# Optimization experiments

Measured on AMD Instinct MI355X. Metric: run time of the kernel, lower is better.

## Reference

```python
import jax, jax.numpy as jnp
import numpy as np

EPS = 1e-5

def mean_variance_norm(x):
    # x: [b,c,h,w]; torch .var(dim=2) on flattened spatial is UNBIASED (n-1)
    b, c, h, w = x.shape
    n = h * w
    mean = jnp.mean(x, axis=(2, 3), keepdims=True)
    var = jnp.sum((x - mean) ** 2, axis=(2, 3), keepdims=True) / (n - 1) + EPS
    return (x - mean) / jnp.sqrt(var)

def conv1x1(x, W, b):
    # 1x1 conv == channel-mixing matmul. W: [out_c, in_c], b: [out_c]
    return jnp.einsum('oc,bchw->bohw', W, x) + b[None, :, None, None]

def setup_inputs() -> dict:
    key = jax.random.key(0)
    ks = jax.random.split(key, 10)
    C = 512
    shp = (4, C, 64, 64)
    std = 1.0 / np.sqrt(C)
    return {
        'content': jax.random.normal(ks[0], shp, jnp.float32),
        'style': jax.random.normal(ks[1], shp, jnp.float32),
        'Wf': jax.random.normal(ks[2], (C, C), jnp.float32) * std,
        'bf': jax.random.normal(ks[3], (C,), jnp.float32) * 0.01,
        'Wg': jax.random.normal(ks[4], (C, C), jnp.float32) * std,
        'bg': jax.random.normal(ks[5], (C,), jnp.float32) * 0.01,
        'Wh': jax.random.normal(ks[6], (C, C), jnp.float32) * std,
        'bh': jax.random.normal(ks[7], (C,), jnp.float32) * 0.01,
        'Wo': jax.random.normal(ks[8], (C, C), jnp.float32) * std,
        'bo': jax.random.normal(ks[9], (C,), jnp.float32) * 0.01,
    }

def reference(content, style, Wf, bf, Wg, bg, Wh, bh, Wo, bo):
    b, c, h, w = content.shape
    hw = h * w
    F = conv1x1(mean_variance_norm(content), Wf, bf).reshape(b, c, hw)  # queries
    G = conv1x1(mean_variance_norm(style), Wg, bg).reshape(b, c, hw)    # keys
    H = conv1x1(style, Wh, bh).reshape(b, c, hw)                        # values
    # S[b,n,m] = sum_c F[b,c,n] * G[b,c,m]  (unscaled attention scores)
    S = jnp.einsum('bcn,bcm->bnm', F, G)
    S = jax.nn.softmax(S, axis=-1)
    # O[b,c,n] = sum_m H[b,c,m] * S[b,n,m]
    O = jnp.einsum('bcm,bnm->bcn', H, S).reshape(b, c, h, w)
    O = conv1x1(O, Wo, bo)
    return O + content
```

## Files before the change

### kernel.cpp

```cpp
#include <hip/hip_runtime.h>

#define C 512
#define HW 4096
#define EPSV 1e-5f

typedef _Float16 fp16x8 __attribute__((ext_vector_type(8)));
typedef _Float16 fp16x4 __attribute__((ext_vector_type(4)));
typedef float f32x4 __attribute__((ext_vector_type(4)));

#define OFF_MC    (0)
#define OFF_RC    (8192)
#define OFF_MS    (16384)
#define OFF_RS    (24576)
#define OFF_BETAF (32768)
#define OFF_V     (40960)
#define OFF_BZ    (49152)
#define OFF_T     (65536)
#define OFF_SP    (131072)
#define OFF_A     (OFF_SP + 2097152)
#define OFF_WZ    (OFF_A + 1048576)
#define OFF_XCT   (OFF_WZ + 1048576)
#define OFF_XST   (OFF_XCT + 16777216)
#define OFF_KT    (OFF_XST + 16777216)
#define OFF_HM    (OFF_KT + 16777216)
#define OFF_ML    (OFF_HM + 16777216)
#define OFF_S     (OFF_ML + 8388608)

#define FT_IDX(n, c) ((((size_t)((n) >> 4) * 16 + ((c) >> 5)) * 512) + \
                      ((((c) >> 3) & 3) * 128) + (((n) & 15) * 8) + ((c) & 7))

#define SFT_IDX(n, m) ((((size_t)((n) >> 4) * 128 + ((m) >> 5)) * 512) + \
                       ((((m) >> 3) & 3) * 128) + (((n) & 15) * 8) + ((m) & 7))



__global__ void transpose_stats_kernel(const float* __restrict__ xc, const float* __restrict__ xs,
                                       char* __restrict__ ws)
{
    int bx = blockIdx.x;
    int tensor = bx >> 11, b = (bx >> 9) & 3, c0 = ((bx >> 6) & 7) * 64, n0 = (bx & 63) * 64;
    const float* src = tensor ? xs : xc;
    _Float16* dst = (_Float16*)(ws + (tensor ? OFF_XST : OFF_XCT));
    float2* part = (float2*)(ws + OFF_SP);

    __shared__ _Float16 tile[64][72];
    __shared__ float pS[64][16], pSS[64][16];

    int tid = threadIdx.x, w = tid >> 6, lane = tid & 63, cq = lane >> 4, l16 = lane & 15;
    #pragma unroll
    for (int k = 0; k < 4; k++) {
        int cr = w * 16 + k * 4 + cq;
        int nf = l16 * 4;
        float4 v = *(const float4*)(src + ((size_t)(b * C + c0 + cr)) * HW + n0 + nf);
        pS[cr][l16] = v.x + v.y + v.z + v.w;
        pSS[cr][l16] = v.x * v.x + v.y * v.y + v.z * v.z + v.w * v.w;
        tile[nf][cr] = (_Float16)v.x; tile[nf + 1][cr] = (_Float16)v.y;
        tile[nf + 2][cr] = (_Float16)v.z; tile[nf + 3][cr] = (_Float16)v.w;
    }
    __syncthreads();
    if (tid < 64) {
        float S = 0.f, SS = 0.f;
        #pragma unroll
        for (int j = 0; j < 16; j++) { S += pS[tid][j]; SS += pSS[tid][j]; }
        part[((size_t)(n0 >> 6)) * 4096 + (tensor * 4 + b) * 512 + c0 + tid] =
            make_float2(S, SS);
    }
    _Float16* dstB = dst + (size_t)b * HW * C;
    #pragma unroll
    for (int i = 0; i < 2; i++) {
        int g = tid + i * 256, row = g >> 3, c8 = (g & 7) * 8;
        int n = n0 + row, c = c0 + c8;
        *(fp16x8*)&dstB[FT_IDX(n, c)] = *(const fp16x8*)&tile[row][c8];
    }
}

__global__ void finalize_stats_kernel(char* __restrict__ ws)
{
    int ch = blockIdx.x * 256 + threadIdx.x;
    const float2* part = (const float2*)(ws + OFF_SP);
    float S = 0.f, SS = 0.f;
    for (int k = 0; k < 64; k++) { float2 v = part[(size_t)k * 4096 + ch]; S += v.x; SS += v.y; }
    int tensor = ch >> 11, rem = ch & 2047;
    float m = S / (float)HW;
    float var = (SS - S * m) / (float)(HW - 1) + EPSV;
    ((float*)(ws + (tensor ? OFF_MS : OFF_MC)))[rem] = m;
    ((float*)(ws + (tensor ? OFF_RS : OFF_RC)))[rem] = rsqrtf(var);
}

__global__ void precompute_kernel(const float* __restrict__ Wf, const float* __restrict__ Wg,
                                  const float* __restrict__ Wo, const float* __restrict__ Wh,
                                  char* __restrict__ ws)
{
    float* A = (float*)(ws + OFF_A);
    _Float16* Wz16 = (_Float16*)(ws + OFF_WZ);
    int bx = blockIdx.x, t = threadIdx.x;
    bool isA = bx < 256;
    int r0 = (isA ? bx : bx - 256) * 2;
    float a00 = 0.f, a01 = 0.f, a10 = 0.f, a11 = 0.f;
    for (int k = 0; k < C; k++) {
        float r0v, r1v, c0v, c1v;
        if (isA) {
            r0v = Wf[k * C + r0]; r1v = Wf[k * C + r0 + 1];
            c0v = Wg[k * C + t];  c1v = Wg[k * C + t + 256];
        } else {
            r0v = Wo[r0 * C + k]; r1v = Wo[(r0 + 1) * C + k];
            c0v = Wh[k * C + t];  c1v = Wh[k * C + t + 256];
        }
        a00 += r0v * c0v; a01 += r0v * c1v;
        a10 += r1v * c0v; a11 += r1v * c1v;
    }
    if (isA) {
        A[r0 * C + t] = a00;       A[r0 * C + t + 256] = a01;
        A[(r0 + 1) * C + t] = a10; A[(r0 + 1) * C + t + 256] = a11;
    } else {
        Wz16[FT_IDX(r0, t)] = (_Float16)a00;
        Wz16[FT_IDX(r0, t + 256)] = (_Float16)a01;
        Wz16[FT_IDX(r0 + 1, t)] = (_Float16)a10;
        Wz16[FT_IDX(r0 + 1, t + 256)] = (_Float16)a11;
    }
}

__global__ void __launch_bounds__(256) vecprep_kernel(const float* __restrict__ Wf,
                                                      const float* __restrict__ bf,
                                                      const float* __restrict__ Wo,
                                                      const float* __restrict__ bh,
                                                      char* __restrict__ ws)
{
    const float* mc = (const float*)(ws + OFF_MC);
    const float* rc = (const float*)(ws + OFF_RC);
    float* betaf = (float*)(ws + OFF_BETAF);
    float* bz = (float*)(ws + OFF_BZ);

    int o = blockIdx.x * 4 + (threadIdx.x >> 6);
    int lane = threadIdx.x & 63;
    float acc = 0.f;
    if (o < 2048) {
        int b = o >> 9, co = o & 511;
        const float* wr = Wf + (size_t)co * C + lane * 8;
        const float* mp = mc + b * C + lane * 8;
        const float* rp = rc + b * C + lane * 8;
        #pragma unroll
        for (int e = 0; e < 8; e++) acc += wr[e] * mp[e] * rp[e];
    } else {
        int co = o - 2048;
        const float* wr = Wo + (size_t)co * C + lane * 8;
        const float* bp = bh + lane * 8;
        #pragma unroll
        for (int e = 0; e < 8; e++) acc += wr[e] * bp[e];
    }
    acc += __shfl_xor(acc, 1);
    acc += __shfl_xor(acc, 2);
    acc += __shfl_xor(acc, 4);
    acc += __shfl_xor(acc, 8);
    acc += __shfl_xor(acc, 16);
    acc += __shfl_xor(acc, 32);
    if (lane == 0) {
        if (o < 2048) betaf[o] = bf[o & 511] - acc;
        else bz[o - 2048] = acc;
    }
}

__global__ void __launch_bounds__(256) scaleA_kernel(char* __restrict__ ws)
{
    const float* __restrict__ A = (const float*)(ws + OFF_A);
    const float* __restrict__ rc = (const float*)(ws + OFF_RC);
    const float* __restrict__ rs = (const float*)(ws + OFF_RS);
    _Float16* __restrict__ As = (_Float16*)(ws + OFF_SP);

    __shared__ float At[16][516];
    __shared__ float rsl[512];
    __shared__ float rcl[16];

    int bx = blockIdx.x;
    int b = bx >> 5, r16 = bx & 31;
    int r0 = r16 * 16;
    int t = threadIdx.x;

    rsl[t] = rs[b * C + t];
    rsl[t + 256] = rs[b * C + t + 256];
    if (t < 16) rcl[t] = rc[b * C + r0 + t];
    {
        int row = t >> 4, cb = (t & 15) * 32;
        const float* src = A + (size_t)(r0 + row) * C + cb;
        #pragma unroll
        for (int k = 0; k < 8; k++) {
            float4 v = *(const float4*)(src + k * 4);
            At[row][cb + k * 4] = v.x; At[row][cb + k * 4 + 1] = v.y;
            At[row][cb + k * 4 + 2] = v.z; At[row][cb + k * 4 + 3] = v.w;
        }
    }
    __syncthreads();

    _Float16* AsB = As + (size_t)b * 262144 + (size_t)r16 * 8192;
    #pragma unroll
    for (int round = 0; round < 4; round++) {
        int flat = round * 2048 + t * 8;
        int cb4 = flat >> 9, rem = flat & 511;
        int low6 = rem >> 3;
        int q = low6 >> 4, l16 = low6 & 15;
        int cbase = cb4 * 32 + q * 8;
        float rcv = rcl[l16];
        fp16x8 o;
        #pragma unroll
        for (int e = 0; e < 8; e++)
            o[e] = (_Float16)(At[l16][cbase + e] * rcv * rsl[cbase + e]);
        *(fp16x8*)&AsB[flat] = o;
    }
}

__global__ void __launch_bounds__(256) precompute_v_kernel(const float* __restrict__ Wg,
                                                           char* __restrict__ ws)
{
    const float* betaf = (const float*)(ws + OFF_BETAF);
    const float* rs = (const float*)(ws + OFF_RS);
    float* v = (float*)(ws + OFF_V);

    __shared__ float bet[512];
    __shared__ float Wgt[64][68];
    __shared__ float pacc[4][64];
    __shared__ float rsl[64];

    int bx = blockIdx.x;
    int b = bx >> 3, j0 = (bx & 7) * 64;
    int t = threadIdx.x;

    bet[t] = betaf[b * C + t];
    bet[t + 256] = betaf[b * C + t + 256];
    if (t < 64) rsl[t] = rs[b * C + j0 + t];

    int j = t & 63, g = t >> 6;
    float acc = 0.f;
    for (int ch = 0; ch < 8; ch++) {
        __syncthreads();
        {
            int row = t >> 2, cq = (t & 3) * 16;
            const float* src = Wg + (size_t)(ch * 64 + row) * C + j0 + cq;
            #pragma unroll
            for (int k = 0; k < 4; k++) {
                float4 w4 = *(const float4*)(src + k * 4);
                Wgt[row][cq + k * 4] = w4.x; Wgt[row][cq + k * 4 + 1] = w4.y;
                Wgt[row][cq + k * 4 + 2] = w4.z; Wgt[row][cq + k * 4 + 3] = w4.w;
            }
        }
        __syncthreads();
        #pragma unroll
        for (int r2 = 0; r2 < 16; r2++) {
            int col = g * 16 + r2;
            acc += bet[ch * 64 + col] * Wgt[col][j];
        }
    }
    pacc[g][j] = acc;
    __syncthreads();
    if (t < 64)
        v[b * C + j0 + t] = rsl[t] * (pacc[0][t] + pacc[1][t] + pacc[2][t] + pacc[3][t]);
}

__global__ void __launch_bounds__(256) prep_gemm_kernel(char* __restrict__ ws)
{
    const _Float16* __restrict__ As = (const _Float16*)(ws + OFF_SP);
    const _Float16* __restrict__ Wz16 = (const _Float16*)(ws + OFF_WZ);
    const float* __restrict__ bz = (const float*)(ws + OFF_BZ);
    const _Float16* __restrict__ xsT = (const _Float16*)(ws + OFF_XST);
    _Float16* __restrict__ Kt = (_Float16*)(ws + OFF_KT);
    _Float16* __restrict__ Hp = (_Float16*)(ws + OFF_HM);

    int bx = blockIdx.x;
    int b = bx & 3, rest = bx >> 2;
    int r128 = rest >> 5, mb = rest & 31;
    int r0 = r128 * 128, m0 = mb * 128;
    int w = threadIdx.x >> 6, lane = threadIdx.x & 63, q = lane >> 4, l16 = lane & 15;
    int wr = (w & 1) * 64, wm = (w >> 1) * 64;
    bool isK = (r0 < 512);
    int rbase = (isK ? r0 : r0 - 512) + wr;

    f32x4 zz = {0.f, 0.f, 0.f, 0.f};
    f32x4 acc[4][4];
    #pragma unroll
    for (int rt = 0; rt < 4; rt++)
        #pragma unroll
        for (int mt = 0; mt < 4; mt++) acc[rt][mt] = zz;

    const _Float16* ap = (isK ? As + (size_t)b * 262144 : Wz16)
                         + (size_t)(rbase >> 4) * 8192 + q * 128 + l16 * 8;
    const _Float16* xb = xsT + (size_t)b * HW * C
                             + (size_t)((m0 + wm) >> 4) * 8192 + q * 128 + l16 * 8;

    for (int ks = 0; ks < 16; ks++) {
        fp16x8 afr[4], bfr[4];
        #pragma unroll
        for (int rt = 0; rt < 4; rt++)
            afr[rt] = *(const fp16x8*)(ap + (size_t)rt * 8192 + ks * 512);
        #pragma unroll
        for (int mt = 0; mt < 4; mt++)
            bfr[mt] = *(const fp16x8*)(xb + (size_t)(mt * 16 + ks) * 512);
        #pragma unroll
        for (int rt = 0; rt < 4; rt++)
            #pragma unroll
            for (int mt = 0; mt < 4; mt++)
                acc[rt][mt] = __builtin_amdgcn_mfma_f32_16x16x32_f16(afr[rt], bfr[mt], acc[rt][mt], 0, 0, 0);
    }

    if (isK) {
        _Float16* KtB = Kt + (size_t)b * HW * C;
        #pragma unroll
        for (int rt = 0; rt < 4; rt++)
            #pragma unroll
            for (int mt = 0; mt < 4; mt++) {
                int m = m0 + wm + mt * 16 + l16;
                int cb = r0 + wr + rt * 16 + q * 4;
                fp16x4 h;
                h[0] = (_Float16)acc[rt][mt][0]; h[1] = (_Float16)acc[rt][mt][1];
                h[2] = (_Float16)acc[rt][mt][2]; h[3] = (_Float16)acc[rt][mt][3];
                *(fp16x4*)&KtB[FT_IDX(m, cb)] = h;
            }
    } else {
        _Float16* HpB = Hp + (size_t)b * 2097152;
        #pragma unroll
        for (int rt = 0; rt < 4; rt++) {
            float bzv[4];
            #pragma unroll
            for (int reg = 0; reg < 4; reg++) bzv[reg] = bz[rbase + rt * 16 + q * 4 + reg];
            #pragma unroll
            for (int mt = 0; mt < 4; mt++) {
                int m = m0 + wm + mt * 16 + l16;
                int mbase = (m >> 3) * 128 + (m & 7);
                #pragma unroll
                for (int reg = 0; reg < 4; reg++) {
                    int co = rbase + rt * 16 + q * 4 + reg;
                    HpB[(size_t)(co >> 4) * 65536 + mbase + (co & 15) * 8] =
                        (_Float16)(acc[rt][mt][reg] + bzv[reg]);
                }
            }
        }
    }
}

__global__ void t_kernel(char* __restrict__ ws)
{
    const float* v = (const float*)(ws + OFF_V);
    const _Float16* __restrict__ xsT = (const _Float16*)(ws + OFF_XST);
    float* tG = (float*)(ws + OFF_T);
    int bx = blockIdx.x;
    int b = bx >> 6, mb = bx & 63;
    int tid = threadIdx.x, w = tid >> 6, lane = tid & 63, q = lane >> 4, l16 = lane & 15;
    int M16 = mb * 4 + w;
    const _Float16* p = xsT + (size_t)b * HW * C + (size_t)M16 * 8192 + q * 128 + l16 * 8;
    const float* vp = v + b * C + q * 8;
    float acc = 0.f;
    #pragma unroll
    for (int st = 0; st < 16; st++) {
        fp16x8 xv = *(const fp16x8*)(p + st * 512);
        float4 v0 = *(const float4*)(vp + st * 32);
        float4 v1 = *(const float4*)(vp + st * 32 + 4);
        acc += (float)xv[0] * v0.x + (float)xv[1] * v0.y + (float)xv[2] * v0.z + (float)xv[3] * v0.w
             + (float)xv[4] * v1.x + (float)xv[5] * v1.y + (float)xv[6] * v1.z + (float)xv[7] * v1.w;
    }
    acc += __shfl_xor(acc, 16);
    acc += __shfl_xor(acc, 32);
    if (q == 0) tG[b * HW + M16 * 16 + l16] = acc;
}

__global__ void __launch_bounds__(256, 4) qk_kernel(char* __restrict__ ws)
{
    const _Float16* __restrict__ xcT = (const _Float16*)(ws + OFF_XCT);
    const _Float16* __restrict__ Kt = (const _Float16*)(ws + OFF_KT);
    const float* __restrict__ tG = (const float*)(ws + OFF_T);
    float2* __restrict__ ML = (float2*)(ws + OFF_ML);
    _Float16* __restrict__ Sg = (_Float16*)(ws + OFF_S);

    int bx = blockIdx.x;
    int b = (bx >> 1) & 3, mhi = bx & 1;
    int rest = bx >> 3, mlo = rest & 15, ntile = rest >> 4;
    int m0 = (mhi * 16 + mlo) * 128, n0 = ntile * 128;
    int tid = threadIdx.x, w = tid >> 6, lane = tid & 63, q = lane >> 4, l16 = lane & 15;
    int wn = (w & 1) * 64, wm = (w >> 1) * 64;

    __shared__ char lbuf[36864];
    _Float16* Ax0 = (_Float16*)lbuf;
    _Float16* Bx0 = (_Float16*)(lbuf + 16384);

    int st = tid >> 5, so = (tid & 31) * 16;
    const _Float16* gA = xcT + (size_t)b * HW * C + ((size_t)(n0 >> 4) + st) * 8192 + so;
    const _Float16* gB = Kt + (size_t)b * HW * C + ((size_t)(m0 >> 4) + st) * 8192 + so;

    {
        fp16x8 a0 = *(const fp16x8*)(gA);
        fp16x8 a1 = *(const fp16x8*)(gA + 8);
        fp16x8 b0 = *(const fp16x8*)(gB);
        fp16x8 b1 = *(const fp16x8*)(gB + 8);
        *(fp16x8*)&Ax0[tid * 16] = a0; *(fp16x8*)&Ax0[tid * 16 + 8] = a1;
        *(fp16x8*)&Bx0[tid * 16] = b0; *(fp16x8*)&Bx0[tid * 16 + 8] = b1;
    }
    __syncthreads();

    f32x4 zz = {0.f, 0.f, 0.f, 0.f};
    f32x4 acc[4][4];
    #pragma unroll
    for (int nt = 0; nt < 4; nt++)
        #pragma unroll
        for (int mt = 0; mt < 4; mt++) acc[nt][mt] = zz;

    int aoff = ((wn >> 4)) * 512 + q * 128 + l16 * 8;
    int boff = ((wm >> 4)) * 512 + q * 128 + l16 * 8;

    for (int ks = 0; ks < 16; ks++) {
        int buf = ks & 1;
        _Float16* Axc = Ax0 + buf * 4096;
        _Float16* Bxc = Bx0 + buf * 4096;
        fp16x8 a0n, a1n, b0n, b1n;
        if (ks < 15) {
            a0n = *(const fp16x8*)(gA + (ks + 1) * 512);
            a1n = *(const fp16x8*)(gA + (ks + 1) * 512 + 8);
            b0n = *(const fp16x8*)(gB + (ks + 1) * 512);
            b1n = *(const fp16x8*)(gB + (ks + 1) * 512 + 8);
        }

        fp16x8 afr[4], bfr[4];
        #pragma unroll
        for (int nt = 0; nt < 4; nt++)
            afr[nt] = *(const fp16x8*)&Axc[aoff + nt * 512];
        #pragma unroll
        for (int mt = 0; mt < 4; mt++)
            bfr[mt] = *(const fp16x8*)&Bxc[boff + mt * 512];
        #pragma unroll
        for (int nt = 0; nt < 4; nt++)
            #pragma unroll
            for (int mt = 0; mt < 4; mt++)
                acc[nt][mt] = __builtin_amdgcn_mfma_f32_16x16x32_f16(afr[nt], bfr[mt], acc[nt][mt], 0, 0, 0);

        if (ks < 15) {
            _Float16* Axn = Ax0 + (buf ^ 1) * 4096;
            _Float16* Bxn = Bx0 + (buf ^ 1) * 4096;
            *(fp16x8*)&Axn[tid * 16] = a0n; *(fp16x8*)&Axn[tid * 16 + 8] = a1n;
            *(fp16x8*)&Bxn[tid * 16] = b0n; *(fp16x8*)&Bxn[tid * 16 + 8] = b1n;
        }
        __syncthreads();
    }

    float tv[4];
    #pragma unroll
    for (int mt = 0; mt < 4; mt++) tv[mt] = tG[b * HW + m0 + wm + mt * 16 + l16];
    #pragma unroll
    for (int nt = 0; nt < 4; nt++)
        #pragma unroll
        for (int mt = 0; mt < 4; mt++)
            #pragma unroll
            for (int reg = 0; reg < 4; reg++) acc[nt][mt][reg] += tv[mt];

    float rm[4][4], sum[4][4];
    #pragma unroll
    for (int nt = 0; nt < 4; nt++)
        #pragma unroll
        for (int reg = 0; reg < 4; reg++)
            rm[nt][reg] = fmaxf(fmaxf(acc[nt][0][reg], acc[nt][1][reg]),
                                fmaxf(acc[nt][2][reg], acc[nt][3][reg]));
    #pragma unroll
    for (int s = 1; s < 16; s <<= 1)
        #pragma unroll
        for (int nt = 0; nt < 4; nt++)
            #pragma unroll
            for (int reg = 0; reg < 4; reg++)
                rm[nt][reg] = fmaxf(rm[nt][reg], __shfl_xor(rm[nt][reg], s));
    #pragma unroll
    for (int nt = 0; nt < 4; nt++)
        #pragma unroll
        for (int reg = 0; reg < 4; reg++) sum[nt][reg] = 0.f;
    #pragma unroll
    for (int nt = 0; nt < 4; nt++)
        #pragma unroll
        for (int mt = 0; mt < 4; mt++)
            #pragma unroll
            for (int reg = 0; reg < 4; reg++) {
                float pv = __expf(acc[nt][mt][reg] - rm[nt][reg]);
                acc[nt][mt][reg] = pv;
                sum[nt][reg] += pv;
            }
    #pragma unroll
    for (int s = 1; s < 16; s <<= 1)
        #pragma unroll
        for (int nt = 0; nt < 4; nt++)
            #pragma unroll
            for (int reg = 0; reg < 4; reg++)
                sum[nt][reg] += __shfl_xor(sum[nt][reg], s);

    int tl = (m0 + wm) >> 6;
    if (l16 == 0) {
        #pragma unroll
        for (int nt = 0; nt < 4; nt++)
            #pragma unroll
            for (int reg = 0; reg < 4; reg++)
                ML[((size_t)(b * HW + n0 + wn + nt * 16 + q * 4 + reg)) * 64 + tl] =
                    make_float2(rm[nt][reg], sum[nt][reg]);
    }

    _Float16 (*Pl)[64][72] = (_Float16(*)[64][72])lbuf;
    #pragma unroll
    for (int nt = 0; nt < 4; nt++)
        #pragma unroll
        for (int mt = 0; mt < 4; mt++)
            #pragma unroll
            for (int reg = 0; reg < 4; reg++)
                Pl[w][nt * 16 + q * 4 + reg][mt * 16 + l16] = (_Float16)acc[nt][mt][reg];
    __syncthreads();
    _Float16* SgB = Sg + (size_t)b * 16777216;
    #pragma unroll
    for (int i = 0; i < 8; i++) {
        int row = i * 8 + (lane >> 3), c8 = (lane & 7) * 8;
        int n = n0 + wn + row, m = m0 + wm + c8;
        *(fp16x8*)&SgB[SFT_IDX(n, m)] = *(const fp16x8*)&Pl[w][row][c8];
    }
}

__global__ void __launch_bounds__(256) scale_kernel(char* __restrict__ ws)
{
    const float* __restrict__ mlf0 = (const float*)(ws + OFF_ML);
    float* __restrict__ Scl = (float*)(ws + OFF_XCT);
    __shared__ float mlv[64][129];
    __shared__ float Ms[64], Li[64];

    int g0 = blockIdx.x * 64;
    int tid = threadIdx.x;
    const float* mlf = mlf0 + (size_t)g0 * 128;

    #pragma unroll
    for (int i = 0; i < 8; i++) {
        int f4 = i * 256 + tid;
        int row = f4 >> 5, c4 = (f4 & 31) * 4;
        float4 v = *(const float4*)(mlf + row * 128 + c4);
        mlv[row][c4] = v.x; mlv[row][c4 + 1] = v.y;
        mlv[row][c4 + 2] = v.z; mlv[row][c4 + 3] = v.w;
    }
    __syncthreads();
    if (tid < 64) {
        float M = -1e30f;
        #pragma unroll
        for (int k = 0; k < 64; k++) M = fmaxf(M, mlv[tid][k * 2]);
        float L = 0.f;
        #pragma unroll
        for (int k = 0; k < 64; k++) L += mlv[tid][k * 2 + 1] * __expf(mlv[tid][k * 2] - M);
        Ms[tid] = M; Li[tid] = 1.f / L;
    }
    __syncthreads();
    int b = g0 >> 12, nbase = g0 & 4095;
    float* sp = Scl + (size_t)b * 262144 + nbase;
    int row = tid & 63, tsub = tid >> 6;
    #pragma unroll
    for (int pass = 0; pass < 16; pass++) {
        int tile = pass * 4 + tsub;
        sp[(size_t)tile * 4096 + row] = __expf(mlv[row][tile * 2] - Ms[row]) * Li[row];
    }
}

__global__ void __launch_bounds__(256, 4) pv_kernel(const float* __restrict__ xc,
                                                    const float* __restrict__ bo,
                                                    float* __restrict__ out,
                                                    char* __restrict__ ws)
{
    const _Float16* __restrict__ Sft = (const _Float16*)(ws + OFF_S);
    const _Float16* __restrict__ Hp = (const _Float16*)(ws + OFF_HM);
    const float* __restrict__ Scl = (const float*)(ws + OFF_XCT);

    int bx = blockIdx.x;
    int b = bx & 3, cog = (bx >> 2) & 7, ntb = bx >> 5;
    int co0 = cog * 64;
    int tid = threadIdx.x, w = tid >> 6, lane = tid & 63, q = lane >> 4, l16 = lane & 15;
    int n0w = ntb * 128 + w * 32;

    __shared__ _Float16 Hl[2][4096];

    int ln64 = lane;
    const _Float16* hsrc = Hp + (size_t)b * 2097152
                              + (size_t)((co0 >> 4) + w) * 65536 + ln64 * 8;
    const _Float16* sb = Sft + (size_t)b * 16777216
                             + (size_t)(ntb * 8 + w * 2) * 65536 + q * 128 + l16 * 8;
    const float* sc = Scl + (size_t)b * 262144 + n0w + q * 4;

    {
        fp16x8 s0 = *(const fp16x8*)(hsrc);
        fp16x8 s1 = *(const fp16x8*)(hsrc + 512);
        *(fp16x8*)&Hl[0][w * 1024 + ln64 * 8] = s0;
        *(fp16x8*)&Hl[0][w * 1024 + 512 + ln64 * 8] = s1;
    }
    __syncthreads();

    f32x4 zz = {0.f, 0.f, 0.f, 0.f};
    f32x4 acc[2][4];
    #pragma unroll
    for (int nt = 0; nt < 2; nt++)
        #pragma unroll
        for (int ct = 0; ct < 4; ct++) acc[nt][ct] = zz;

    for (int chunk = 0; chunk < 64; chunk++) {
        int buf = chunk & 1;
        fp16x8 s0n, s1n;
        if (chunk < 63) {
            s0n = *(const fp16x8*)(hsrc + (chunk + 1) * 1024);
            s1n = *(const fp16x8*)(hsrc + (chunk + 1) * 1024 + 512);
        }

        f32x4 tmp[2][4];
        #pragma unroll
        for (int km = 0; km < 2; km++) {
            fp16x8 afr[2], bfr[4];
            #pragma unroll
            for (int nt = 0; nt < 2; nt++)
                afr[nt] = *(const fp16x8*)(sb + (size_t)nt * 65536 + (chunk * 2 + km) * 512);
            #pragma unroll
            for (int ct = 0; ct < 4; ct++)
                bfr[ct] = *(const fp16x8*)&Hl[buf][ct * 1024 + (km * 4 + q) * 128 + l16 * 8];
            #pragma unroll
            for (int nt = 0; nt < 2; nt++)
                #pragma unroll
                for (int ct = 0; ct < 4; ct++)
                    tmp[nt][ct] = __builtin_amdgcn_mfma_f32_16x16x32_f16(
                        afr[nt], bfr[km == 0 ? ct : ct], km == 0 ? zz : tmp[nt][ct], 0, 0, 0);
        }
        float4 sv0 = *(const float4*)(sc + chunk * 4096);
        float4 sv1 = *(const float4*)(sc + chunk * 4096 + 16);
        float sva[2][4] = {{sv0.x, sv0.y, sv0.z, sv0.w}, {sv1.x, sv1.y, sv1.z, sv1.w}};
        #pragma unroll
        for (int nt = 0; nt < 2; nt++)
            #pragma unroll
            for (int ct = 0; ct < 4; ct++)
                #pragma unroll
                for (int reg = 0; reg < 4; reg++)
                    acc[nt][ct][reg] += tmp[nt][ct][reg] * sva[nt][reg];

        if (chunk < 63) {
            *(fp16x8*)&Hl[buf ^ 1][w * 1024 + ln64 * 8] = s0n;
            *(fp16x8*)&Hl[buf ^ 1][w * 1024 + 512 + ln64 * 8] = s1n;
        }
        __syncthreads();
    }

    #pragma unroll
    for (int nt = 0; nt < 2; nt++)
        #pragma unroll
        for (int ct = 0; ct < 4; ct++) {
            int co = co0 + ct * 16 + l16;
            size_t base = ((size_t)(b * C + co)) * HW + n0w + nt * 16 + q * 4;
            float4 cv = *(const float4*)&xc[base];
            float bov = bo[co];
            float4 o;
            o.x = acc[nt][ct][0] + bov + cv.x;
            o.y = acc[nt][ct][1] + bov + cv.y;
            o.z = acc[nt][ct][2] + bov + cv.z;
            o.w = acc[nt][ct][3] + bov + cv.w;
            *(float4*)&out[base] = o;
        }
}

extern "C" void kernel_launch(void* const* d_in, const int* in_sizes, int n_in,
                              void* d_out, int out_size, void* d_ws, size_t ws_size,
                              hipStream_t stream)
{
    const float* content = (const float*)d_in[0];
    const float* style   = (const float*)d_in[1];
    const float* Wf = (const float*)d_in[2];
    const float* bf = (const float*)d_in[3];
    const float* Wg = (const float*)d_in[4];
    const float* Wh = (const float*)d_in[6];
    const float* bh = (const float*)d_in[7];
    const float* Wo = (const float*)d_in[8];
    const float* bo = (const float*)d_in[9];
    float* out = (float*)d_out;
    char* ws = (char*)d_ws;

    transpose_stats_kernel<<<4096, 256, 0, stream>>>(content, style, ws);
    finalize_stats_kernel<<<16, 256, 0, stream>>>(ws);
    precompute_kernel<<<512, 256, 0, stream>>>(Wf, Wg, Wo, Wh, ws);
    vecprep_kernel<<<640, 256, 0, stream>>>(Wf, bf, Wo, bh, ws);
    scaleA_kernel<<<128, 256, 0, stream>>>(ws);
    precompute_v_kernel<<<32, 256, 0, stream>>>(Wg, ws);
    prep_gemm_kernel<<<1024, 256, 0, stream>>>(ws);
    t_kernel<<<256, 256, 0, stream>>>(ws);
    qk_kernel<<<4096, 256, 0, stream>>>(ws);
    scale_kernel<<<256, 256, 0, stream>>>(ws);
    pv_kernel<<<1024, 256, 0, stream>>>(content, bo, out, ws);
}
```

Baseline: 474.7 us.

## Merge independent prep kernels and fold softmax rescale into PV kernel

```diff
diff --git a/kernel.cpp b/kernel.cpp
--- a/kernel.cpp
+++ b/kernel.cpp
@@ -74,28 +74,30 @@
     }
 }
 
-__global__ void finalize_stats_kernel(char* __restrict__ ws)
-{
-    int ch = blockIdx.x * 256 + threadIdx.x;
-    const float2* part = (const float2*)(ws + OFF_SP);
-    float S = 0.f, SS = 0.f;
-    for (int k = 0; k < 64; k++) { float2 v = part[(size_t)k * 4096 + ch]; S += v.x; SS += v.y; }
-    int tensor = ch >> 11, rem = ch & 2047;
-    float m = S / (float)HW;
-    float var = (SS - S * m) / (float)(HW - 1) + EPSV;
-    ((float*)(ws + (tensor ? OFF_MS : OFF_MC)))[rem] = m;
-    ((float*)(ws + (tensor ? OFF_RS : OFF_RC)))[rem] = rsqrtf(var);
-}
-
-__global__ void precompute_kernel(const float* __restrict__ Wf, const float* __restrict__ Wg,
-                                  const float* __restrict__ Wo, const float* __restrict__ Wh,
-                                  char* __restrict__ ws)
-{
+__global__ void __launch_bounds__(256) stage1_kernel(const float* __restrict__ Wf,
+                                                     const float* __restrict__ Wg,
+                                                     const float* __restrict__ Wo,
+                                                     const float* __restrict__ Wh,
+                                                     char* __restrict__ ws)
+{
+    int bx = blockIdx.x, t = threadIdx.x;
+    if (bx < 16) {
+        int ch = bx * 256 + t;
+        const float2* part = (const float2*)(ws + OFF_SP);
+        float S = 0.f, SS = 0.f;
+        for (int k = 0; k < 64; k++) { float2 v = part[(size_t)k * 4096 + ch]; S += v.x; SS += v.y; }
+        int tensor = ch >> 11, rem = ch & 2047;
+        float m = S / (float)HW;
+        float var = (SS - S * m) / (float)(HW - 1) + EPSV;
+        ((float*)(ws + (tensor ? OFF_MS : OFF_MC)))[rem] = m;
+        ((float*)(ws + (tensor ? OFF_RS : OFF_RC)))[rem] = rsqrtf(var);
+        return;
+    }
     float* A = (float*)(ws + OFF_A);
     _Float16* Wz16 = (_Float16*)(ws + OFF_WZ);
-    int bx = blockIdx.x, t = threadIdx.x;
-    bool isA = bx < 256;
-    int r0 = (isA ? bx : bx - 256) * 2;
+    int bx2 = bx - 16;
+    bool isA = bx2 < 256;
+    int r0 = (isA ? bx2 : bx2 - 256) * 2;
     float a00 = 0.f, a01 = 0.f, a10 = 0.f, a11 = 0.f;
     for (int k = 0; k < C; k++) {
         float r0v, r1v, c0v, c1v;
@@ -120,91 +122,91 @@
     }
 }
 
-__global__ void __launch_bounds__(256) vecprep_kernel(const float* __restrict__ Wf,
-                                                      const float* __restrict__ bf,
-                                                      const float* __restrict__ Wo,
-                                                      const float* __restrict__ bh,
-                                                      char* __restrict__ ws)
-{
-    const float* mc = (const float*)(ws + OFF_MC);
-    const float* rc = (const float*)(ws + OFF_RC);
-    float* betaf = (float*)(ws + OFF_BETAF);
-    float* bz = (float*)(ws + OFF_BZ);
-
-    int o = blockIdx.x * 4 + (threadIdx.x >> 6);
-    int lane = threadIdx.x & 63;
-    float acc = 0.f;
-    if (o < 2048) {
-        int b = o >> 9, co = o & 511;
-        const float* wr = Wf + (size_t)co * C + lane * 8;
-        const float* mp = mc + b * C + lane * 8;
-        const float* rp = rc + b * C + lane * 8;
-        #pragma unroll
-        for (int e = 0; e < 8; e++) acc += wr[e] * mp[e] * rp[e];
-    } else {
-        int co = o - 2048;
-        const float* wr = Wo + (size_t)co * C + lane * 8;
-        const float* bp = bh + lane * 8;
-        #pragma unroll
-        for (int e = 0; e < 8; e++) acc += wr[e] * bp[e];
-    }
-    acc += __shfl_xor(acc, 1);
-    acc += __shfl_xor(acc, 2);
-    acc += __shfl_xor(acc, 4);
-    acc += __shfl_xor(acc, 8);
-    acc += __shfl_xor(acc, 16);
-    acc += __shfl_xor(acc, 32);
-    if (lane == 0) {
-        if (o < 2048) betaf[o] = bf[o & 511] - acc;
-        else bz[o - 2048] = acc;
-    }
-}
-
-__global__ void __launch_bounds__(256) scaleA_kernel(char* __restrict__ ws)
-{
-    const float* __restrict__ A = (const float*)(ws + OFF_A);
-    const float* __restrict__ rc = (const float*)(ws + OFF_RC);
-    const float* __restrict__ rs = (const float*)(ws + OFF_RS);
-    _Float16* __restrict__ As = (_Float16*)(ws + OFF_SP);
-
+__global__ void __launch_bounds__(256) stage2_kernel(const float* __restrict__ Wf,
+                                                     const float* __restrict__ bf,
+                                                     const float* __restrict__ Wo,
+                                                     const float* __restrict__ bh,
+                                                     char* __restrict__ ws)
+{
     __shared__ float At[16][516];
     __shared__ float rsl[512];
     __shared__ float rcl[16];
 
-    int bx = blockIdx.x;
-    int b = bx >> 5, r16 = bx & 31;
-    int r0 = r16 * 16;
-    int t = threadIdx.x;
-
-    rsl[t] = rs[b * C + t];
-    rsl[t + 256] = rs[b * C + t + 256];
-    if (t < 16) rcl[t] = rc[b * C + r0 + t];
+    int bx = blockIdx.x, t = threadIdx.x;
+    if (bx < 640) {
+        const float* mc = (const float*)(ws + OFF_MC);
+        const float* rc = (const float*)(ws + OFF_RC);
+        float* betaf = (float*)(ws + OFF_BETAF);
+        float* bz = (float*)(ws + OFF_BZ);
+        int o = bx * 4 + (t >> 6);
+        int lane = t & 63;
+        float acc = 0.f;
+        if (o < 2048) {
+            int b = o >> 9, co = o & 511;
+            const float* wr = Wf + (size_t)co * C + lane * 8;
+            const float* mp = mc + b * C + lane * 8;
+            const float* rp = rc + b * C + lane * 8;
+            #pragma unroll
+            for (int e = 0; e < 8; e++) acc += wr[e] * mp[e] * rp[e];
+        } else {
+            int co = o - 2048;
+            const float* wr = Wo + (size_t)co * C + lane * 8;
+            const float* bp = bh + lane * 8;
+            #pragma unroll
+            for (int e = 0; e < 8; e++) acc += wr[e] * bp[e];
+        }
+        acc += __shfl_xor(acc, 1);
+        acc += __shfl_xor(acc, 2);
+        acc += __shfl_xor(acc, 4);
+        acc += __shfl_xor(acc, 8);
+        acc += __shfl_xor(acc, 16);
+        acc += __shfl_xor(acc, 32);
+        if (lane == 0) {
+            if (o < 2048) betaf[o] = bf[o & 511] - acc;
+            else bz[o - 2048] = acc;
+        }
+        return;
+    }
     {
-        int row = t >> 4, cb = (t & 15) * 32;
-        const float* src = A + (size_t)(r0 + row) * C + cb;
-        #pragma unroll
-        for (int k = 0; k < 8; k++) {
-            float4 v = *(const float4*)(src + k * 4);
-            At[row][cb + k * 4] = v.x; At[row][cb + k * 4 + 1] = v.y;
-            At[row][cb + k * 4 + 2] = v.z; At[row][cb + k * 4 + 3] = v.w;
-        }
-    }
-    __syncthreads();
-
-    _Float16* AsB = As + (size_t)b * 262144 + (size_t)r16 * 8192;
-    #pragma unroll
-    for (int round = 0; round < 4; round++) {
-        int flat = round * 2048 + t * 8;
-        int cb4 = flat >> 9, rem = flat & 511;
-        int low6 = rem >> 3;
-        int q = low6 >> 4, l16 = low6 & 15;
-        int cbase = cb4 * 32 + q * 8;
-        float rcv = rcl[l16];
-        fp16x8 o;
-        #pragma unroll
-        for (int e = 0; e < 8; e++)
-            o[e] = (_Float16)(At[l16][cbase + e] * rcv * rsl[cbase + e]);
-        *(fp16x8*)&AsB[flat] = o;
+        const float* __restrict__ A = (const float*)(ws + OFF_A);
+        const float* __restrict__ rc = (const float*)(ws + OFF_RC);
+        const float* __restrict__ rs = (const float*)(ws + OFF_RS);
+        _Float16* __restrict__ As = (_Float16*)(ws + OFF_SP);
+
+        int bx2 = bx - 640;
+        int b = bx2 >> 5, r16 = bx2 & 31;
+        int r0 = r16 * 16;
+
+        rsl[t] = rs[b * C + t];
+        rsl[t + 256] = rs[b * C + t + 256];
+        if (t < 16) rcl[t] = rc[b * C + r0 + t];
+        {
+            int row = t >> 4, cb = (t & 15) * 32;
+            const float* src = A + (size_t)(r0 + row) * C + cb;
+            #pragma unroll
+            for (int k = 0; k < 8; k++) {
+                float4 v = *(const float4*)(src + k * 4);
+                At[row][cb + k * 4] = v.x; At[row][cb + k * 4 + 1] = v.y;
+                At[row][cb + k * 4 + 2] = v.z; At[row][cb + k * 4 + 3] = v.w;
+            }
+        }
+        __syncthreads();
+
+        _Float16* AsB = As + (size_t)b * 262144 + (size_t)r16 * 8192;
+        #pragma unroll
+        for (int round = 0; round < 4; round++) {
+            int flat = round * 2048 + t * 8;
+            int cb4 = flat >> 9, rem = flat & 511;
+            int low6 = rem >> 3;
+            int q = low6 >> 4, l16 = low6 & 15;
+            int cbase = cb4 * 32 + q * 8;
+            float rcv = rcl[l16];
+            fp16x8 o;
+            #pragma unroll
+            for (int e = 0; e < 8; e++)
+                o[e] = (_Float16)(At[l16][cbase + e] * rcv * rsl[cbase + e]);
+            *(fp16x8*)&AsB[flat] = o;
+        }
     }
 }
 
@@ -255,8 +257,32 @@
         v[b * C + j0 + t] = rsl[t] * (pacc[0][t] + pacc[1][t] + pacc[2][t] + pacc[3][t]);
 }
 
-__global__ void __launch_bounds__(256) prep_gemm_kernel(char* __restrict__ ws)
-{
+__global__ void __launch_bounds__(256) stage4_kernel(char* __restrict__ ws)
+{
+    if (blockIdx.x >= 1024) {
+        const float* v = (const float*)(ws + OFF_V);
+        const _Float16* __restrict__ xsT = (const _Float16*)(ws + OFF_XST);
+        float* tG = (float*)(ws + OFF_T);
+        int bx2 = blockIdx.x - 1024;
+        int b = bx2 >> 6, mb = bx2 & 63;
+        int tid = threadIdx.x, w = tid >> 6, lane = tid & 63, q = lane >> 4, l16 = lane & 15;
+        int M16 = mb * 4 + w;
+        const _Float16* p = xsT + (size_t)b * HW * C + (size_t)M16 * 8192 + q * 128 + l16 * 8;
+        const float* vp = v + b * C + q * 8;
+        float acc = 0.f;
+        #pragma unroll
+        for (int st = 0; st < 16; st++) {
+            fp16x8 xv = *(const fp16x8*)(p + st * 512);
+            float4 v0 = *(const float4*)(vp + st * 32);
+            float4 v1 = *(const float4*)(vp + st * 32 + 4);
+            acc += (float)xv[0] * v0.x + (float)xv[1] * v0.y + (float)xv[2] * v0.z + (float)xv[3] * v0.w
+                 + (float)xv[4] * v1.x + (float)xv[5] * v1.y + (float)xv[6] * v1.z + (float)xv[7] * v1.w;
+        }
+        acc += __shfl_xor(acc, 16);
+        acc += __shfl_xor(acc, 32);
+        if (q == 0) tG[b * HW + M16 * 16 + l16] = acc;
+        return;
+    }
     const _Float16* __restrict__ As = (const _Float16*)(ws + OFF_SP);
     const _Float16* __restrict__ Wz16 = (const _Float16*)(ws + OFF_WZ);
     const float* __restrict__ bz = (const float*)(ws + OFF_BZ);
@@ -335,31 +361,6 @@
     }
 }
 
-__global__ void t_kernel(char* __restrict__ ws)
-{
-    const float* v = (const float*)(ws + OFF_V);
-    const _Float16* __restrict__ xsT = (const _Float16*)(ws + OFF_XST);
-    float* tG = (float*)(ws + OFF_T);
-    int bx = blockIdx.x;
-    int b = bx >> 6, mb = bx & 63;
-    int tid = threadIdx.x, w = tid >> 6, lane = tid & 63, q = lane >> 4, l16 = lane & 15;
-    int M16 = mb * 4 + w;
-    const _Float16* p = xsT + (size_t)b * HW * C + (size_t)M16 * 8192 + q * 128 + l16 * 8;
-    const float* vp = v + b * C + q * 8;
-    float acc = 0.f;
-    #pragma unroll
-    for (int st = 0; st < 16; st++) {
-        fp16x8 xv = *(const fp16x8*)(p + st * 512);
-        float4 v0 = *(const float4*)(vp + st * 32);
-        float4 v1 = *(const float4*)(vp + st * 32 + 4);
-        acc += (float)xv[0] * v0.x + (float)xv[1] * v0.y + (float)xv[2] * v0.z + (float)xv[3] * v0.w
-             + (float)xv[4] * v1.x + (float)xv[5] * v1.y + (float)xv[6] * v1.z + (float)xv[7] * v1.w;
-    }
-    acc += __shfl_xor(acc, 16);
-    acc += __shfl_xor(acc, 32);
-    if (q == 0) tG[b * HW + M16 * 16 + l16] = acc;
-}
-
 __global__ void __launch_bounds__(256, 4) qk_kernel(char* __restrict__ ws)
 {
     const _Float16* __restrict__ xcT = (const _Float16*)(ws + OFF_XCT);
@@ -511,46 +512,6 @@
     }
 }
 
-__global__ void __launch_bounds__(256) scale_kernel(char* __restrict__ ws)
-{
-    const float* __restrict__ mlf0 = (const float*)(ws + OFF_ML);
-    float* __restrict__ Scl = (float*)(ws + OFF_XCT);
-    __shared__ float mlv[64][129];
-    __shared__ float Ms[64], Li[64];
-
-    int g0 = blockIdx.x * 64;
-    int tid = threadIdx.x;
-    const float* mlf = mlf0 + (size_t)g0 * 128;
-
-    #pragma unroll
-    for (int i = 0; i < 8; i++) {
-        int f4 = i * 256 + tid;
-        int row = f4 >> 5, c4 = (f4 & 31) * 4;
-        float4 v = *(const float4*)(mlf + row * 128 + c4);
-        mlv[row][c4] = v.x; mlv[row][c4 + 1] = v.y;
-        mlv[row][c4 + 2] = v.z; mlv[row][c4 + 3] = v.w;
-    }
-    __syncthreads();
-    if (tid < 64) {
-        float M = -1e30f;
-        #pragma unroll
-        for (int k = 0; k < 64; k++) M = fmaxf(M, mlv[tid][k * 2]);
-        float L = 0.f;
-        #pragma unroll
-        for (int k = 0; k < 64; k++) L += mlv[tid][k * 2 + 1] * __expf(mlv[tid][k * 2] - M);
-        Ms[tid] = M; Li[tid] = 1.f / L;
-    }
-    __syncthreads();
-    int b = g0 >> 12, nbase = g0 & 4095;
-    float* sp = Scl + (size_t)b * 262144 + nbase;
-    int row = tid & 63, tsub = tid >> 6;
-    #pragma unroll
-    for (int pass = 0; pass < 16; pass++) {
-        int tile = pass * 4 + tsub;
-        sp[(size_t)tile * 4096 + row] = __expf(mlv[row][tile * 2] - Ms[row]) * Li[row];
-    }
-}
-
 __global__ void __launch_bounds__(256, 4) pv_kernel(const float* __restrict__ xc,
                                                     const float* __restrict__ bo,
                                                     float* __restrict__ out,
@@ -558,7 +519,7 @@
 {
     const _Float16* __restrict__ Sft = (const _Float16*)(ws + OFF_S);
     const _Float16* __restrict__ Hp = (const _Float16*)(ws + OFF_HM);
-    const float* __restrict__ Scl = (const float*)(ws + OFF_XCT);
+    const float2* __restrict__ ML = (const float2*)(ws + OFF_ML);
 
     int bx = blockIdx.x;
     int b = bx & 3, cog = (bx >> 2) & 7, ntb = bx >> 5;
@@ -567,13 +528,40 @@
     int n0w = ntb * 128 + w * 32;
 
     __shared__ _Float16 Hl[2][4096];
+    __shared__ _Float16 SclH[64][132];
+
+    {
+        int row = tid >> 1, part = tid & 1;
+        const float2* mlp = ML + ((size_t)(b * HW + ntb * 128 + row)) * 64 + part * 32;
+        float M = -1e30f;
+        #pragma unroll
+        for (int k = 0; k < 32; k += 4) {
+            float4 a = *(const float4*)(mlp + k);
+            float4 c = *(const float4*)(mlp + k + 2);
+            M = fmaxf(M, fmaxf(fmaxf(a.x, a.z), fmaxf(c.x, c.z)));
+        }
+        M = fmaxf(M, __shfl_xor(M, 1));
+        float L = 0.f;
+        #pragma unroll
+        for (int k = 0; k < 32; k += 2) {
+            float4 a = *(const float4*)(mlp + k);
+            L += a.y * __expf(a.x - M) + a.w * __expf(a.z - M);
+        }
+        L += __shfl_xor(L, 1);
+        float linv = 1.f / L;
+        #pragma unroll
+        for (int k = 0; k < 32; k += 2) {
+            float4 a = *(const float4*)(mlp + k);
+            SclH[part * 32 + k][row] = (_Float16)(__expf(a.x - M) * linv);
+            SclH[part * 32 + k + 1][row] = (_Float16)(__expf(a.z - M) * linv);
+        }
+    }
 
     int ln64 = lane;
     const _Float16* hsrc = Hp + (size_t)b * 2097152
                               + (size_t)((co0 >> 4) + w) * 65536 + ln64 * 8;
     const _Float16* sb = Sft + (size_t)b * 16777216
                              + (size_t)(ntb * 8 + w * 2) * 65536 + q * 128 + l16 * 8;
-    const float* sc = Scl + (size_t)b * 262144 + n0w + q * 4;
 
     {
         fp16x8 s0 = *(const fp16x8*)(hsrc);
@@ -613,11 +601,12 @@
                 #pragma unroll
                 for (int ct = 0; ct < 4; ct++)
                     tmp[nt][ct] = __builtin_amdgcn_mfma_f32_16x16x32_f16(
-                        afr[nt], bfr[km == 0 ? ct : ct], km == 0 ? zz : tmp[nt][ct], 0, 0, 0);
-        }
-        float4 sv0 = *(const float4*)(sc + chunk * 4096);
-        float4 sv1 = *(const float4*)(sc + chunk * 4096 + 16);
-        float sva[2][4] = {{sv0.x, sv0.y, sv0.z, sv0.w}, {sv1.x, sv1.y, sv1.z, sv1.w}};
+                        afr[nt], bfr[ct], km == 0 ? zz : tmp[nt][ct], 0, 0, 0);
+        }
+        fp16x4 svh0 = *(const fp16x4*)&SclH[chunk][w * 32 + q * 4];
+        fp16x4 svh1 = *(const fp16x4*)&SclH[chunk][w * 32 + 16 + q * 4];
+        float sva[2][4] = {{(float)svh0[0], (float)svh0[1], (float)svh0[2], (float)svh0[3]},
+                           {(float)svh1[0], (float)svh1[1], (float)svh1[2], (float)svh1[3]}};
         #pragma unroll
         for (int nt = 0; nt < 2; nt++)
             #pragma unroll
@@ -667,14 +656,10 @@
     char* ws = (char*)d_ws;
 
     transpose_stats_kernel<<<4096, 256, 0, stream>>>(content, style, ws);
-    finalize_stats_kernel<<<16, 256, 0, stream>>>(ws);
-    precompute_kernel<<<512, 256, 0, stream>>>(Wf, Wg, Wo, Wh, ws);
-    vecprep_kernel<<<640, 256, 0, stream>>>(Wf, bf, Wo, bh, ws);
-    scaleA_kernel<<<128, 256, 0, stream>>>(ws);
+    stage1_kernel<<<528, 256, 0, stream>>>(Wf, Wg, Wo, Wh, ws);
+    stage2_kernel<<<768, 256, 0, stream>>>(Wf, bf, Wo, bh, ws);
     precompute_v_kernel<<<32, 256, 0, stream>>>(Wg, ws);
-    prep_gemm_kernel<<<1024, 256, 0, stream>>>(ws);
-    t_kernel<<<256, 256, 0, stream>>>(ws);
+    stage4_kernel<<<1280, 256, 0, stream>>>(ws);
     qk_kernel<<<4096, 256, 0, stream>>>(ws);
-    scale_kernel<<<256, 256, 0, stream>>>(ws);
     pv_kernel<<<1024, 256, 0, stream>>>(content, bo, out, ws);
 }
```

After: 471.7 us. No clear change (-0.6%).
